# Kernel optimization log

Hardware: AMD Instinct MI355X
Metric: run time of the kernel (lower is better)

The kernel has to match this reference:

```python
import jax, jax.numpy as jnp
import numpy as np

B, C_IN, C_OUT, C_KEY, N = 8, 512, 512, 256, 2048


def setup_inputs() -> dict:
    key = jax.random.key(0)
    k1, k2, k3, k4 = jax.random.split(key, 4)
    x = jax.random.normal(k1, (B, C_IN, N), dtype=jnp.float32)
    # Conv1d(kernel=1, bias=False) weights -> plain linear maps over channel dim
    Wq = jax.random.normal(k2, (C_KEY, C_IN), dtype=jnp.float32) * (1.0 / np.sqrt(C_IN))
    Wk = jax.random.normal(k3, (C_KEY, C_IN), dtype=jnp.float32) * (1.0 / np.sqrt(C_IN))
    Wv = jax.random.normal(k4, (C_OUT, C_IN), dtype=jnp.float32) * (1.0 / np.sqrt(C_IN))
    return {"x": x, "Wq": Wq, "Wk": Wk, "Wv": Wv}


def reference(x, Wq, Wk, Wv):
    # 1x1 conv projections: [B, C, N] -> [B, Ck/Co, N]
    q = jnp.einsum("oc,bcn->bon", Wq, x)
    k = jnp.einsum("oc,bcn->bon", Wk, x)
    v = jnpqv = jnp.einsum("oc,bcn->bon", Wv, x)
    # sim_map[b,i,j] = sum_c k[b,c,i] * q[b,c,j]  (unscaled)
    sim = jnp.einsum("bci,bcj->bij", k, q)  # [B, N, N]
    attn = jax.nn.softmax(sim, axis=-1)
    # out = value @ sim_map, then permute(0,2,1) -> [B, N, C_out]
    out = jnp.einsum("bck,bkm->bmc", jnpqv, attn)
    return out
```

## Files before the change

### kernel.cpp

```cpp
#include <hip/hip_runtime.h>

typedef _Float16 half8 __attribute__((ext_vector_type(8)));
typedef _Float16 half4v __attribute__((ext_vector_type(4)));
typedef _Float16 half2v __attribute__((ext_vector_type(2)));
typedef float f32x4 __attribute__((ext_vector_type(4)));

#define ASYNC_CP16(gp, lp)                                       \
  __builtin_amdgcn_global_load_lds(                              \
      (const __attribute__((address_space(1))) void*)(gp),       \
      (__attribute__((address_space(3))) void*)(lp), 16, 0, 0)

static __device__ __forceinline__ half8 mulw(half8 a, half8 s) {
  half8 o;
#pragma unroll
  for (int j = 0; j < 8; j++) o[j] = a[j] * s[j];
  return o;
}

__global__ __launch_bounds__(256) void conv_w(const float* __restrict__ Wq,
                                              const float* __restrict__ Wk,
                                              const float* __restrict__ Wv,
                                              _Float16* __restrict__ Wb) {
  int idx = blockIdx.x * 256 + threadIdx.x;
  int row = idx >> 9;
  float v;
  if (row < 256)      v = Wq[idx];
  else if (row < 512) v = Wk[idx - 256 * 512];
  else                v = Wv[idx - 512 * 512];
  Wb[idx] = (_Float16)v;
}

__global__ __launch_bounds__(256) void conv_xT(const float* __restrict__ x,
                                               _Float16* __restrict__ xT) {
  __shared__ float T[32][33];
  const int b = blockIdx.z;
  const int n0 = blockIdx.x * 32, c0 = blockIdx.y * 32;
  const int t = threadIdx.x;
  const float* xb = x + (size_t)b * 512 * 2048;
  const int n2 = t & 15, cr = t >> 4;
#pragma unroll
  for (int r = 0; r < 2; r++) {
    int c = cr + r * 16;
    float2 v = *(const float2*)&xb[(size_t)(c0 + c) * 2048 + n0 + n2 * 2];
    T[c][n2 * 2] = v.x;
    T[c][n2 * 2 + 1] = v.y;
  }
  __syncthreads();
  _Float16* xtb = xT + (size_t)b * 2048 * 512;
  const int c2 = t & 15, nr = t >> 4;
#pragma unroll
  for (int r = 0; r < 2; r++) {
    int n = nr + r * 16;
    half2v h;
    h[0] = (_Float16)T[c2 * 2][n];
    h[1] = (_Float16)T[c2 * 2 + 1][n];
    *(half2v*)&xtb[(size_t)(n0 + n) * 512 + c0 + c2 * 2] = h;
  }
}

template <typename OutT, int BUFS, int MODE>
__global__ __launch_bounds__(256) void gemm_nt(
    const _Float16* __restrict__ A, const _Float16* __restrict__ B,
    OutT* __restrict__ C, OutT* __restrict__ C2, int K, int lda, int ldb,
    int ldc, int ldc2, long sA, long sB, long sC, float* __restrict__ pm,
    float* __restrict__ ps) {
  A += (size_t)blockIdx.z * sA;
  B += (size_t)blockIdx.z * sB;
  C += (size_t)blockIdx.z * sC;
  if constexpr (MODE == 1) C2 += (size_t)blockIdx.z * sC;
  const int m_blk = blockIdx.y * 128, n_blk = blockIdx.x * 128;

  __shared__ __align__(16) _Float16 As[BUFS][4096];
  __shared__ __align__(16) _Float16 Bs[BUFS][4096];

  const int t = threadIdx.x;
  const int lane = t & 63, wave = t >> 6;
  const int quad = lane >> 4, l16 = lane & 15;
  const int wm = (wave & 1) * 64, wn = (wave >> 1) * 64;

  const int srow = 16 * wave + (lane >> 2);
  const int schunk = (lane & 3) ^ ((lane >> 3) & 3);
  const _Float16* gA0 = A + (size_t)(m_blk + srow) * lda + schunk * 8;
  const _Float16* gA1 = gA0 + (size_t)64 * lda;
  const _Float16* gB0 = B + (size_t)(n_blk + srow) * ldb + schunk * 8;
  const _Float16* gB1 = gB0 + (size_t)64 * ldb;
  const int lofs = wave * 512 + lane * 8;

  const int rchunk = (quad ^ ((l16 >> 1) & 3)) * 8;

  f32x4 acc[4][4] = {};

#pragma unroll
  for (int pb = 0; pb < BUFS - 1; pb++) {
    if (pb * 32 < K) {
      ASYNC_CP16(gA0 + pb * 32, &As[pb][lofs]);
      ASYNC_CP16(gA1 + pb * 32, &As[pb][lofs + 2048]);
      ASYNC_CP16(gB0 + pb * 32, &Bs[pb][lofs]);
      ASYNC_CP16(gB1 + pb * 32, &Bs[pb][lofs + 2048]);
    }
  }

  int ib = 0;
  for (int k0 = 0; k0 < K; k0 += 32) {
    if constexpr (BUFS == 3) {
      if (k0 + 32 < K)
        asm volatile("s_waitcnt vmcnt(4)\n\ts_barrier" ::: "memory");
      else
        asm volatile("s_waitcnt vmcnt(0)\n\ts_barrier" ::: "memory");
    } else {
      asm volatile("s_waitcnt vmcnt(0)\n\ts_barrier" ::: "memory");
    }
    if (k0 + (BUFS - 1) * 32 < K) {
      int nb = ib + BUFS - 1;
      if (nb >= BUFS) nb -= BUFS;
      const int ko = k0 + (BUFS - 1) * 32;
      ASYNC_CP16(gA0 + ko, &As[nb][lofs]);
      ASYNC_CP16(gA1 + ko, &As[nb][lofs + 2048]);
      ASYNC_CP16(gB0 + ko, &Bs[nb][lofs]);
      ASYNC_CP16(gB1 + ko, &Bs[nb][lofs + 2048]);
    }
    half8 af[4], bf[4];
#pragma unroll
    for (int i = 0; i < 4; i++) {
      af[i] = *(const half8*)&As[ib][(wm + i * 16 + l16) * 32 + rchunk];
      bf[i] = *(const half8*)&Bs[ib][(wn + i * 16 + l16) * 32 + rchunk];
    }
#pragma unroll
    for (int i = 0; i < 4; i++)
#pragma unroll
      for (int j = 0; j < 4; j++)
        acc[i][j] =
            __builtin_amdgcn_mfma_f32_16x16x32_f16(af[i], bf[j], acc[i][j], 0, 0, 0);
    ib++;
    if (ib == BUFS) ib = 0;
  }

  if constexpr (MODE == 2) {
#pragma unroll
    for (int j = 0; j < 4; j++) {
      const int n0 = n_blk + wn + j * 16 + l16;
      float mx = acc[0][j][0];
#pragma unroll
      for (int i = 0; i < 4; i++)
#pragma unroll
        for (int r = 0; r < 4; r++) mx = fmaxf(mx, acc[i][j][r]);
      mx = fmaxf(mx, __shfl_xor(mx, 16, 64));
      mx = fmaxf(mx, __shfl_xor(mx, 32, 64));
      float es = 0.f;
#pragma unroll
      for (int i = 0; i < 4; i++) {
        const int m0 = m_blk + wm + i * 16 + quad * 4;
#pragma unroll
        for (int r = 0; r < 4; r++) {
          _Float16 h = (_Float16)__expf(acc[i][j][r] - mx);
          C[(size_t)(m0 + r) * ldc + n0] = h;
          es += (float)h;
        }
      }
      es += __shfl_xor(es, 16, 64);
      es += __shfl_xor(es, 32, 64);
      if (quad == 0) {
        size_t o =
            ((size_t)blockIdx.z * 32 + blockIdx.y * 2 + (wave & 1)) * 2048 + n0;
        pm[o] = mx;
        ps[o] = es;
      }
    }
  } else {
#pragma unroll
    for (int i = 0; i < 4; i++) {
      const int m0 = m_blk + wm + i * 16 + quad * 4;
#pragma unroll
      for (int j = 0; j < 4; j++) {
        const int n0 = n_blk + wn + j * 16 + l16;
        if constexpr (MODE == 1) {
          if (m_blk < 512) {
            half4v h;
#pragma unroll
            for (int r = 0; r < 4; r++) h[r] = (_Float16)acc[i][j][r];
            *(half4v*)&C[(size_t)n0 * ldc + m0] = h;
          } else {
#pragma unroll
            for (int r = 0; r < 4; r++)
              C2[(size_t)(m0 - 512 + r) * ldc2 + n0] = (OutT)acc[i][j][r];
          }
        } else {
#pragma unroll
          for (int r = 0; r < 4; r++)
            C[(size_t)(m0 + r) * ldc + n0] = (OutT)acc[i][j][r];
        }
      }
    }
  }
}

__global__ __launch_bounds__(256) void colstats2(const float* __restrict__ pm,
                                                 const float* __restrict__ ps,
                                                 _Float16* __restrict__ scl) {
  const int idx = blockIdx.x * 256 + threadIdx.x;
  const int b = idx >> 11, col = idx & 2047;
  const float* pmb = pm + (size_t)b * 32 * 2048 + col;
  const float* psb = ps + (size_t)b * 32 * 2048 + col;
  float pv[32];
  float m = -3.0e38f;
#pragma unroll
  for (int i = 0; i < 32; i++) {
    pv[i] = pmb[(size_t)i * 2048];
    m = fmaxf(m, pv[i]);
  }
  float s = 0.f;
#pragma unroll
  for (int i = 0; i < 32; i++) {
    pv[i] = __expf(pv[i] - m);
    s += psb[(size_t)i * 2048] * pv[i];
  }
  const float inv = 1.0f / s;
  _Float16* so = scl + (size_t)b * 32 * 2048 + col;
#pragma unroll
  for (int i = 0; i < 32; i++) so[(size_t)i * 2048] = (_Float16)(pv[i] * inv);
}

__global__ __launch_bounds__(512) void gemm_av(const _Float16* __restrict__ P,
                                               const _Float16* __restrict__ V,
                                               const _Float16* __restrict__ scl,
                                               float* __restrict__ C,
                                               int cbatch) {
  int lin = blockIdx.x, z, idx;
  if (cbatch == 8) {
    z = lin & 7;
    idx = lin >> 3;
  } else {
    z = lin >> 5;
    idx = lin & 31;
  }
  const int n_blk = (idx & 1) * 256;
  const int m_blk = (idx >> 1) * 128;
  P += (size_t)z * 2048 * 2048;
  V += (size_t)z * 512 * 2048;
  scl += (size_t)z * 32 * 2048;
  C += (size_t)z * 2048 * 512;

  __shared__ __align__(16) _Float16 As[2][4096];
  __shared__ __align__(16) _Float16 Bs[3][8192];

  const int t = threadIdx.x;
  const int lane = t & 63, wave = t >> 6;
  const int quad = lane >> 4, l16 = lane & 15;
  const int wm = (wave & 1) * 64, wn = (wave >> 1) * 64;

  const int srow = t >> 2;
  const int schunk = (t & 3) ^ ((t >> 3) & 3);
  const _Float16* gA = P + (size_t)(m_blk + srow) * 2048 + schunk * 8;
  const _Float16* gS =
      scl + (size_t)((m_blk + srow) >> 6) * 2048 + schunk * 8;
  const _Float16* gB0 = V + (size_t)(n_blk + srow) * 2048 + schunk * 8;
  const _Float16* gB1 = gB0 + (size_t)128 * 2048;
  const int lofs = t * 8;
  const int rchunk = (quad ^ ((l16 >> 1) & 3)) * 8;

  f32x4 acc[4][4] = {};

  ASYNC_CP16(gB0, &Bs[0][lofs]);
  ASYNC_CP16(gB1, &Bs[0][lofs + 4096]);
  ASYNC_CP16(gB0 + 32, &Bs[1][lofs]);
  ASYNC_CP16(gB1 + 32, &Bs[1][lofs + 4096]);
  {
    half8 a0 = *(const half8*)gA;
    half8 s0 = *(const half8*)gS;
    *(half8*)&As[0][lofs] = mulw(a0, s0);
  }
  half8 an0 = *(const half8*)(gA + 32);
  half8 sn0 = *(const half8*)(gS + 32);
  asm volatile("s_waitcnt vmcnt(0)\n\ts_barrier" ::: "memory");

  int ibA = 0, ibB = 0;
  for (int k0 = 0; k0 < 2048; k0 += 32) {
    const bool m1 = (k0 + 32 < 2048), m2 = (k0 + 64 < 2048);
    if (m2) {
      int nb = ibB + 2;
      if (nb >= 3) nb -= 3;
      ASYNC_CP16(gB0 + k0 + 64, &Bs[nb][lofs]);
      ASYNC_CP16(gB1 + k0 + 64, &Bs[nb][lofs + 4096]);
    }
    half8 a2, s2;
    if (m2) {
      a2 = *(const half8*)(gA + k0 + 64);
      s2 = *(const half8*)(gS + k0 + 64);
    }
    half8 af[4], bf[4];
#pragma unroll
    for (int i = 0; i < 4; i++) {
      af[i] = *(const half8*)&As[ibA][(wm + i * 16 + l16) * 32 + rchunk];
      bf[i] = *(const half8*)&Bs[ibB][(wn + i * 16 + l16) * 32 + rchunk];
    }
#pragma unroll
    for (int i = 0; i < 4; i++)
#pragma unroll
      for (int j = 0; j < 4; j++)
        acc[i][j] =
            __builtin_amdgcn_mfma_f32_16x16x32_f16(af[i], bf[j], acc[i][j], 0, 0, 0);
    if (m1) {
      *(half8*)&As[ibA ^ 1][lofs] = mulw(an0, sn0);
      if (m2) {
        an0 = a2;
        sn0 = s2;
      }
      asm volatile("s_waitcnt vmcnt(4) lgkmcnt(0)\n\ts_barrier" ::: "memory");
    }
    ibA ^= 1;
    ibB++;
    if (ibB == 3) ibB = 0;
  }

#pragma unroll
  for (int i = 0; i < 4; i++) {
    const int m0 = m_blk + wm + i * 16 + quad * 4;
#pragma unroll
    for (int j = 0; j < 4; j++) {
      const int n0 = n_blk + wn + j * 16 + l16;
#pragma unroll
      for (int r = 0; r < 4; r++) C[(size_t)(m0 + r) * 512 + n0] = acc[i][j][r];
    }
  }
}

extern "C" void kernel_launch(void* const* d_in, const int* in_sizes, int n_in,
                              void* d_out, int out_size, void* d_ws,
                              size_t ws_size, hipStream_t stream) {
  const float* x = (const float*)d_in[0];
  const float* Wq = (const float*)d_in[1];
  const float* Wk = (const float*)d_in[2];
  const float* Wv = (const float*)d_in[3];
  float* out = (float*)d_out;

  char* p = (char*)d_ws;
  auto alloc = [&](size_t bytes) -> char* {
    char* r = p;
    p += (bytes + 255) & ~(size_t)255;
    return r;
  };
  const size_t NB = 8, N = 2048, CIN = 512, CO = 512;
  _Float16* Wb = (_Float16*)alloc(1024 * 512 * sizeof(_Float16));
  _Float16* xT = (_Float16*)alloc(NB * N * CIN * sizeof(_Float16));
  _Float16* qkT = (_Float16*)alloc(NB * N * 512 * sizeof(_Float16));
  _Float16* v = (_Float16*)alloc(NB * CO * N * sizeof(_Float16));
  size_t base_used = (size_t)(p - (char*)d_ws);

  const size_t per_b =
      (size_t)N * N * 2 + 2 * 32 * N * 4 + 32 * N * 2 + 8192;
  int cb = 8;
  while (cb > 1 && base_used + (size_t)cb * per_b > ws_size) cb >>= 1;
  _Float16* simH = (_Float16*)alloc((size_t)cb * N * N * 2);
  float* pm = (float*)alloc((size_t)cb * 32 * N * 4);
  float* ps = (float*)alloc((size_t)cb * 32 * N * 4);
  _Float16* scl = (_Float16*)alloc((size_t)cb * 32 * N * 2);

  conv_w<<<dim3(1024 * 512 / 256), 256, 0, stream>>>(Wq, Wk, Wv, Wb);
  conv_xT<<<dim3(64, 16, 8), 256, 0, stream>>>(x, xT);

  gemm_nt<_Float16, 3, 1><<<dim3(16, 8, 8), 256, 0, stream>>>(
      Wb, xT, qkT, v, 512, 512, 512, 512, 2048, 0, (long)(N * CIN),
      (long)(N * 512), nullptr, nullptr);

  for (int b0 = 0; b0 < 8; b0 += cb) {
    const _Float16* qT = qkT + (size_t)b0 * N * 512;
    const _Float16* kT = qkT + (size_t)b0 * N * 512 + 256;
    gemm_nt<_Float16, 2, 2><<<dim3(16, 16, cb), 256, 0, stream>>>(
        qT, kT, simH, nullptr, 256, 512, 512, 2048, 0, (long)(N * 512),
        (long)(N * 512), (long)(N * N), pm, ps);
    colstats2<<<dim3(cb * 8), 256, 0, stream>>>(pm, ps, scl);
    gemm_av<<<dim3(32 * cb), 512, 0, stream>>>(
        simH, v + (size_t)b0 * CO * N, scl, out + (size_t)b0 * N * CO, cb);
  }
}
```

Baseline: 215.8 us.

## Restructure PV GEMM mainloop into 64-wide K steps with ping-pong double buffering

Rewrites the second GEMM's main loop so each iteration processes K=64 as two 32-wide halves. A and B tiles are double-buffered in LDS, replacing the triple-buffered B and double-buffered A. Global-to-LDS loads are remapped per wave with a new swizzle, and the loop adds explicit s_barrier, sched_barrier and s_setprio around the MFMA clusters to interleave memory and compute phases. This aims to cut per-iteration barrier and loop overhead and improve overlap. In exchange it adds more barriers per step and more registers for prefetched data.

```diff
diff --git a/kernel.cpp b/kernel.cpp
--- a/kernel.cpp
+++ b/kernel.cpp
@@ -240,76 +240,113 @@
   scl += (size_t)z * 32 * 2048;
   C += (size_t)z * 2048 * 512;
 
-  __shared__ __align__(16) _Float16 As[2][4096];
-  __shared__ __align__(16) _Float16 Bs[3][8192];
+  __shared__ __align__(16) _Float16 As[2][2][4096];
+  __shared__ __align__(16) _Float16 Bs[2][2][8192];
 
   const int t = threadIdx.x;
   const int lane = t & 63, wave = t >> 6;
   const int quad = lane >> 4, l16 = lane & 15;
   const int wm = (wave & 1) * 64, wn = (wave >> 1) * 64;
 
-  const int srow = t >> 2;
-  const int schunk = (t & 3) ^ ((t >> 3) & 3);
-  const _Float16* gA = P + (size_t)(m_blk + srow) * 2048 + schunk * 8;
-  const _Float16* gS =
-      scl + (size_t)((m_blk + srow) >> 6) * 2048 + schunk * 8;
-  const _Float16* gB0 = V + (size_t)(n_blk + srow) * 2048 + schunk * 8;
-  const _Float16* gB1 = gB0 + (size_t)128 * 2048;
-  const int lofs = t * 8;
+  const int arow = t >> 2;
+  const int aslot = t & 3;
+  const int adc = aslot ^ ((arow >> 1) & 3);
+  const _Float16* gA = P + (size_t)(m_blk + arow) * 2048 + adc * 8;
+  const _Float16* gS = scl + (size_t)((m_blk + arow) >> 6) * 2048 + adc * 8;
+  const int awofs = arow * 32 + aslot * 8;
+
+  const int brow0 = (wave << 4) + (lane >> 2);
+  const int bdc = (lane & 3) ^ ((brow0 >> 1) & 3);
+  const _Float16* gB = V + (size_t)(n_blk + brow0) * 2048 + bdc * 8;
+  const int bwofs = wave << 9;
+
   const int rchunk = (quad ^ ((l16 >> 1) & 3)) * 8;
 
   f32x4 acc[4][4] = {};
 
-  ASYNC_CP16(gB0, &Bs[0][lofs]);
-  ASYNC_CP16(gB1, &Bs[0][lofs + 4096]);
-  ASYNC_CP16(gB0 + 32, &Bs[1][lofs]);
-  ASYNC_CP16(gB1 + 32, &Bs[1][lofs + 4096]);
+  ASYNC_CP16(gB, &Bs[0][0][bwofs]);
+  ASYNC_CP16(gB + (size_t)128 * 2048, &Bs[0][0][4096 + bwofs]);
+  ASYNC_CP16(gB + 32, &Bs[0][1][bwofs]);
+  ASYNC_CP16(gB + (size_t)128 * 2048 + 32, &Bs[0][1][4096 + bwofs]);
   {
-    half8 a0 = *(const half8*)gA;
-    half8 s0 = *(const half8*)gS;
-    *(half8*)&As[0][lofs] = mulw(a0, s0);
-  }
-  half8 an0 = *(const half8*)(gA + 32);
-  half8 sn0 = *(const half8*)(gS + 32);
-  asm volatile("s_waitcnt vmcnt(0)\n\ts_barrier" ::: "memory");
-
-  int ibA = 0, ibB = 0;
-  for (int k0 = 0; k0 < 2048; k0 += 32) {
-    const bool m1 = (k0 + 32 < 2048), m2 = (k0 + 64 < 2048);
-    if (m2) {
-      int nb = ibB + 2;
-      if (nb >= 3) nb -= 3;
-      ASYNC_CP16(gB0 + k0 + 64, &Bs[nb][lofs]);
-      ASYNC_CP16(gB1 + k0 + 64, &Bs[nb][lofs + 4096]);
-    }
-    half8 a2, s2;
-    if (m2) {
-      a2 = *(const half8*)(gA + k0 + 64);
-      s2 = *(const half8*)(gS + k0 + 64);
-    }
+    half8 a00 = *(const half8*)(gA);
+    half8 s00 = *(const half8*)(gS);
+    half8 a01 = *(const half8*)(gA + 32);
+    half8 s01 = *(const half8*)(gS + 32);
+    *(half8*)&As[0][0][awofs] = mulw(a00, s00);
+    *(half8*)&As[0][1][awofs] = mulw(a01, s01);
+  }
+  half8 pA0 = *(const half8*)(gA + 64);
+  half8 pS0 = *(const half8*)(gS + 64);
+  half8 pA1 = *(const half8*)(gA + 96);
+  half8 pS1 = *(const half8*)(gS + 96);
+  asm volatile("s_waitcnt vmcnt(4) lgkmcnt(0)\n\ts_barrier" ::: "memory");
+  __builtin_amdgcn_sched_barrier(0);
+
+  for (int T = 0; T < 32; T++) {
+    const int c = T & 1, n = c ^ 1;
+    const int k1 = (T + 1) * 64;
+    const int k2 = (T + 2) * 64;
     half8 af[4], bf[4];
 #pragma unroll
     for (int i = 0; i < 4; i++) {
-      af[i] = *(const half8*)&As[ibA][(wm + i * 16 + l16) * 32 + rchunk];
-      bf[i] = *(const half8*)&Bs[ibB][(wn + i * 16 + l16) * 32 + rchunk];
-    }
+      af[i] = *(const half8*)&As[c][0][(wm + i * 16 + l16) * 32 + rchunk];
+      bf[i] = *(const half8*)&Bs[c][0][(wn + i * 16 + l16) * 32 + rchunk];
+    }
+    if (T < 31) {
+      ASYNC_CP16(gB + k1, &Bs[n][0][bwofs]);
+      ASYNC_CP16(gB + (size_t)128 * 2048 + k1, &Bs[n][0][4096 + bwofs]);
+      ASYNC_CP16(gB + k1 + 32, &Bs[n][1][bwofs]);
+      ASYNC_CP16(gB + (size_t)128 * 2048 + k1 + 32, &Bs[n][1][4096 + bwofs]);
+      *(half8*)&As[n][0][awofs] = mulw(pA0, pS0);
+    }
+    asm volatile("s_barrier" ::: "memory");
+    __builtin_amdgcn_sched_barrier(0);
+    __builtin_amdgcn_s_setprio(1);
 #pragma unroll
     for (int i = 0; i < 4; i++)
 #pragma unroll
       for (int j = 0; j < 4; j++)
         acc[i][j] =
             __builtin_amdgcn_mfma_f32_16x16x32_f16(af[i], bf[j], acc[i][j], 0, 0, 0);
-    if (m1) {
-      *(half8*)&As[ibA ^ 1][lofs] = mulw(an0, sn0);
-      if (m2) {
-        an0 = a2;
-        sn0 = s2;
-      }
+    __builtin_amdgcn_s_setprio(0);
+    asm volatile("s_barrier" ::: "memory");
+    __builtin_amdgcn_sched_barrier(0);
+    half8 af2[4], bf2[4];
+#pragma unroll
+    for (int i = 0; i < 4; i++) {
+      af2[i] = *(const half8*)&As[c][1][(wm + i * 16 + l16) * 32 + rchunk];
+      bf2[i] = *(const half8*)&Bs[c][1][(wn + i * 16 + l16) * 32 + rchunk];
+    }
+    half8 fA0, fS0, fA1, fS1;
+    if (T < 30) {
+      fA0 = *(const half8*)(gA + k2);
+      fS0 = *(const half8*)(gS + k2);
+      fA1 = *(const half8*)(gA + k2 + 32);
+      fS1 = *(const half8*)(gS + k2 + 32);
+    }
+    if (T < 31) *(half8*)&As[n][1][awofs] = mulw(pA1, pS1);
+    if (T < 30) {
+      pA0 = fA0;
+      pS0 = fS0;
+      pA1 = fA1;
+      pS1 = fS1;
+    }
+    if (T < 30)
       asm volatile("s_waitcnt vmcnt(4) lgkmcnt(0)\n\ts_barrier" ::: "memory");
-    }
-    ibA ^= 1;
-    ibB++;
-    if (ibB == 3) ibB = 0;
+    else
+      asm volatile("s_waitcnt vmcnt(0) lgkmcnt(0)\n\ts_barrier" ::: "memory");
+    __builtin_amdgcn_sched_barrier(0);
+    __builtin_amdgcn_s_setprio(1);
+#pragma unroll
+    for (int i = 0; i < 4; i++)
+#pragma unroll
+      for (int j = 0; j < 4; j++)
+        acc[i][j] =
+            __builtin_amdgcn_mfma_f32_16x16x32_f16(af2[i], bf2[j], acc[i][j], 0, 0, 0);
+    __builtin_amdgcn_s_setprio(0);
+    asm volatile("s_barrier" ::: "memory");
+    __builtin_amdgcn_sched_barrier(0);
   }
 
 #pragma unroll
```

Result: faster. 198.5 us (-8.0%).
